# Optimization experiments

Hardware: AMD Instinct MI355X
Metric: run time of the kernel (lower is better)

The kernel has to match this reference:

```python
import jax, jax.numpy as jnp
import numpy as np

NEG_INF = float("-inf")
WINDOW = 5  # window_size in LocalAttention; half = WINDOW // 2 = 2


def setup_inputs() -> dict:
    key = jax.random.key(0)
    kq, kk, kv = jax.random.split(key, 3)
    B, L, H, E = 4, 2048, 8, 64
    queries = jax.random.normal(kq, (B, L, H, E), dtype=jnp.float32)
    keys = jax.random.normal(kk, (B, L, H, E), dtype=jnp.float32)
    values = jax.random.normal(kv, (B, L, H, E), dtype=jnp.float32)
    return {"queries": queries, "keys": keys, "values": values}


def reference(queries, keys, values):
    # queries/keys/values: [B, L, H, E]; dropout is identity (eval mode).
    B, L, H, E = queries.shape
    scale = 1.0 / jnp.sqrt(jnp.asarray(E, dtype=queries.dtype))
    # Shared scores for both branches: [B, H, L, S]
    scores = jnp.einsum("blhe,bshe->bhls", queries, keys)

    # Global (unmasked) branch
    A_global = jax.nn.softmax(scale * scores, axis=-1)

    # Local branch: torch mask allows j in [max(i-2,0), min(i+2,L)) => i-2 <= j <= i+1
    half = WINDOW // 2
    i = jnp.arange(L)[:, None]
    j = jnp.arange(L)[None, :]
    allowed = (j - i >= -half) & (j - i < half)  # [L, L], asymmetric window
    local_scores = jnp.where(allowed, scores, NEG_INF)
    A_local = jax.nn.softmax(scale * local_scores, axis=-1)

    # Sum of the two attention outputs == (A_global + A_local) @ V
    out = jnp.einsum("bhls,bshd->blhd", A_global + A_local, values)
    return out
```

## Files before the change

### kernel.cpp

```cpp
#include <hip/hip_runtime.h>
#include <hip/hip_bf16.h>
#include <stdint.h>


#define LQ 2048
#define HQ 8
#define EQ 64
#define BQ 4
#define BN 64
#define RS (HQ * EQ)
#define SCALE_LOG2E 0.18033688011112042f
#define NTILE (LQ / BN)
#define TILE_U32 2048
#define IMG_U32 (BQ * HQ * NTILE * TILE_U32)
#define BMQ 64

typedef __attribute__((ext_vector_type(8))) short bf16x8;
typedef __attribute__((ext_vector_type(4))) float f32x4;
typedef __attribute__((ext_vector_type(4))) unsigned int u32x4;
typedef __attribute__((ext_vector_type(2))) unsigned int u32x2;

static __device__ __forceinline__ unsigned int f2bf(float f) {
    union { float f; unsigned int u; } c; c.f = f;
    return (c.u + 0x8000u) >> 16;
}
static __device__ __forceinline__ unsigned int pk2(float lo, float hi) {
    union { float f; unsigned int u; } a, b; a.f = lo; b.f = hi;
    return ((a.u + 0x8000u) >> 16) | ((b.u + 0x8000u) & 0xffff0000u);
}
static __device__ __forceinline__ float fexp2(float x) {
    float r;
    asm volatile("v_exp_f32 %0, %1\n\ts_nop 1" : "=v"(r) : "v"(x));
    return r;
}

__global__ __launch_bounds__(256) void prepack_kernel(
    const float* __restrict__ K, const float* __restrict__ V,
    uint32_t* __restrict__ Kimg, uint32_t* __restrict__ Vimg)
{
    __shared__ float vf[64 * 64];

    const int tid = threadIdx.x;
    const int jc  = blockIdx.x;
    const int bh  = blockIdx.y;
    const int b   = bh >> 3;
    const int h   = bh & 7;
    const int j0  = jc * BN;
    const float* Kbh = K + (size_t)b * LQ * RS + h * EQ;
    const float* Vbh = V + (size_t)b * LQ * RS + h * EQ;
    uint32_t* Kt = Kimg + (size_t)(bh * NTILE + jc) * TILE_U32;
    uint32_t* Vt = Vimg + (size_t)(bh * NTILE + jc) * TILE_U32;

    #pragma unroll
    for (int it = 0; it < 2; ++it) {
        int t2 = tid + it * 256;
        int jr = t2 >> 3, eo = t2 & 7;
        const float* src = Kbh + (size_t)(j0 + jr) * RS + eo * 8;
        float4 a  = *(const float4*)src;
        float4 bv = *(const float4*)(src + 4);
        u32x4 p;
        p.x = pk2(a.x, a.y);   p.y = pk2(a.z, a.w);
        p.z = pk2(bv.x, bv.y); p.w = pk2(bv.z, bv.w);
        *(u32x4*)&Kt[jr * 32 + ((eo ^ (jr & 7)) << 2)] = p;
    }

    {
        const int jr = tid >> 2;
        const int s  = (jr & 7) ^ (jr >> 3);
        const float* src = Vbh + (size_t)(j0 + jr) * RS + (tid & 3) * 16;
        #pragma unroll
        for (int q = 0; q < 4; ++q) {
            float4 a = *(const float4*)(src + q * 4);
            const int ec = (tid & 3) * 4 + q;
            const int p  = (ec & 8) | ((ec ^ s) & 7);
            *(float4*)&vf[jr * 64 + p * 4] = a;
        }
    }
    __syncthreads();

    #pragma unroll
    for (int it = 0; it < 2; ++it) {
        const int u   = tid + it * 256;
        const int e   = u >> 3;
        const int jop = u & 7;
        const int jo  = jop ^ (e & 7);
        const int ec  = e >> 2;
        float v[8];
        #pragma unroll
        for (int k = 0; k < 8; ++k) {
            const int j = jo * 8 + k;
            const int p = (ec & 8) | ((ec ^ (j & 7) ^ (j >> 3)) & 7);
            v[k] = vf[j * 64 + p * 4 + (e & 3)];
        }
        u32x4 pq;
        pq.x = pk2(v[0], v[1]); pq.y = pk2(v[2], v[3]);
        pq.z = pk2(v[4], v[5]); pq.w = pk2(v[6], v[7]);
        *(u32x4*)&Vt[e * 32 + (jop << 2)] = pq;
    }
}

__global__ __launch_bounds__(256, 4) void hybrid_attn_v15(
    const float* __restrict__ Q, const float* __restrict__ K,
    const float* __restrict__ V, const uint32_t* __restrict__ Kimg,
    const uint32_t* __restrict__ Vimg, float* __restrict__ O)
{
    __shared__ unsigned short KV[8192];
    __shared__ unsigned short Pt[4][1024];
    __shared__ float sloc[BMQ][4];

    const int tid  = threadIdx.x;
    const int wave = tid >> 6;
    const int lane = tid & 63;
    const int c    = lane & 15;
    const int g    = lane >> 4;
    const int id   = blockIdx.x;
    const int bh   = (id & 7) * 4 + ((id >> 3) & 3);
    const int qt   = id >> 5;
    const int b    = bh >> 3;
    const int h    = bh & 7;
    const int i0   = qt * BMQ;
    const int c7   = c & 7;
    const int sw3  = c7 << 1;

    const float* Qbh = Q + (size_t)b * LQ * RS + h * EQ;
    const float* Kbh = K + (size_t)b * LQ * RS + h * EQ;
    const float* Vbh = V + (size_t)b * LQ * RS + h * EQ;
    float*       Obh = O + (size_t)b * LQ * RS + h * EQ;

    bf16x8 qf[2];
    {
        const int iq = i0 + wave * 16 + c;
        const float* qrow = Qbh + (size_t)iq * RS + g * 8;
        #pragma unroll
        for (int f = 0; f < 2; ++f) {
            float4 a  = *(const float4*)(qrow + f * 32);
            float4 bv = *(const float4*)(qrow + f * 32 + 4);
            union { bf16x8 v; unsigned int u[4]; } fr;
            fr.u[0] = pk2(a.x  * SCALE_LOG2E, a.y  * SCALE_LOG2E);
            fr.u[1] = pk2(a.z  * SCALE_LOG2E, a.w  * SCALE_LOG2E);
            fr.u[2] = pk2(bv.x * SCALE_LOG2E, bv.y * SCALE_LOG2E);
            fr.u[3] = pk2(bv.z * SCALE_LOG2E, bv.w * SCALE_LOG2E);
            qf[f] = fr.v;
        }
    }

    const int fo0 = c * 64 + ((g ^ c7) << 3);
    const int fo1 = c * 64 + (((4 | g) ^ c7) << 3);

    unsigned short* pw[4];
    #pragma unroll
    for (int n = 0; n < 4; ++n)
        pw[n] = &Pt[wave][c * 64 + ((((n << 2) | g) ^ sw3) << 2)];
    unsigned short* pr0 = &Pt[wave][c * 64 + (((g << 1) ^ sw3) << 2)];
    unsigned short* pr1 = &Pt[wave][c * 64 + (((8 | (g << 1)) ^ sw3) << 2)];

    const uint32_t* kgb = Kimg + (size_t)bh * (NTILE * TILE_U32) + wave * 512 + lane * 4;
    const uint32_t* vgb = Vimg + (size_t)bh * (NTILE * TILE_U32) + wave * 512 + lane * 4;

    unsigned short* kd0 = &KV[wave * 1024 + lane * 8];
    unsigned short* kd1 = &KV[wave * 1024 + 512 + lane * 8];
    unsigned short* vd0 = &KV[4096 + wave * 1024 + lane * 8];
    unsigned short* vd1 = &KV[4096 + wave * 1024 + 512 + lane * 8];

    f32x4 oacc[4];
    #pragma unroll
    for (int eg = 0; eg < 4; ++eg) oacc[eg] = (f32x4){0.f, 0.f, 0.f, 0.f};
    float lsum = 0.f;

    u32x4 kr0 = *(const u32x4*)kgb;
    u32x4 kr1 = *(const u32x4*)(kgb + 256);
    u32x4 vr0 = *(const u32x4*)vgb;
    u32x4 vr1 = *(const u32x4*)(vgb + 256);

    for (int jc = 0; jc < NTILE; ++jc) {
        __syncthreads();
        *(u32x4*)kd0 = kr0;
        *(u32x4*)kd1 = kr1;
        *(u32x4*)vd0 = vr0;
        *(u32x4*)vd1 = vr1;
        if (jc + 1 < NTILE) {
            const uint32_t* kg = kgb + (size_t)(jc + 1) * TILE_U32;
            const uint32_t* vg = vgb + (size_t)(jc + 1) * TILE_U32;
            kr0 = *(const u32x4*)kg;
            kr1 = *(const u32x4*)(kg + 256);
            vr0 = *(const u32x4*)vg;
            vr1 = *(const u32x4*)(vg + 256);
        }
        __syncthreads();

        bf16x8 kfr[4][2];
        #pragma unroll
        for (int n = 0; n < 4; ++n) {
            kfr[n][0] = *(const bf16x8*)&KV[n * 1024 + fo0];
            kfr[n][1] = *(const bf16x8*)&KV[n * 1024 + fo1];
        }

        f32x4 sf[4];
        #pragma unroll
        for (int n = 0; n < 4; ++n) {
            f32x4 acc = (f32x4){0.f, 0.f, 0.f, 0.f};
            acc = __builtin_amdgcn_mfma_f32_16x16x32_bf16(kfr[n][0], qf[0], acc, 0, 0, 0);
            acc = __builtin_amdgcn_mfma_f32_16x16x32_bf16(kfr[n][1], qf[1], acc, 0, 0, 0);
            sf[n] = acc;
        }
        float ls = 0.f;
        #pragma unroll
        for (int n = 0; n < 4; ++n) {
            float p0 = fexp2(sf[n][0]);
            float p1 = fexp2(sf[n][1]);
            float p2 = fexp2(sf[n][2]);
            float p3 = fexp2(sf[n][3]);
            ls += (p0 + p1) + (p2 + p3);
            u32x2 pkd;
            pkd.x = pk2(p0, p1);
            pkd.y = pk2(p2, p3);
            *(u32x2*)pw[n] = pkd;
        }
        lsum += ls;
        asm volatile("s_waitcnt lgkmcnt(0)" ::: "memory");

        bf16x8 pf0 = *(const bf16x8*)pr0;
        bf16x8 pf1 = *(const bf16x8*)pr1;
        #pragma unroll
        for (int eg = 0; eg < 4; ++eg) {
            bf16x8 v0 = *(const bf16x8*)&KV[4096 + eg * 1024 + fo0];
            bf16x8 v1 = *(const bf16x8*)&KV[4096 + eg * 1024 + fo1];
            oacc[eg] = __builtin_amdgcn_mfma_f32_16x16x32_bf16(v0, pf0, oacc[eg], 0, 0, 0);
            oacc[eg] = __builtin_amdgcn_mfma_f32_16x16x32_bf16(v1, pf1, oacc[eg], 0, 0, 0);
        }
    }

    float linv;
    {
        float l = lsum;
        l += __shfl_xor(l, 16);
        l += __shfl_xor(l, 32);
        linv = 1.0f / l;
    }

    {
        const int br = tid >> 2;
        const int jj = tid & 3;
        const int i  = i0 + br;
        const int j  = i - 2 + jj;
        float s = -INFINITY;
        if (j >= 0 && j < LQ) {
            const float* qrow = Qbh + (size_t)i * RS;
            const float* krow = Kbh + (size_t)j * RS;
            float acc = 0.f;
            #pragma unroll
            for (int e = 0; e < 64; e += 4) {
                float4 qa = *(const float4*)(qrow + e);
                float4 ka = *(const float4*)(krow + e);
                acc = fmaf(qa.x, ka.x, acc); acc = fmaf(qa.y, ka.y, acc);
                acc = fmaf(qa.z, ka.z, acc); acc = fmaf(qa.w, ka.w, acc);
            }
            s = 0.125f * acc;
        }
        sloc[br][jj] = s;
    }
    __syncthreads();

    {
        const int row = wave * 16 + c;
        const int i   = i0 + row;
        float s0 = sloc[row][0], s1 = sloc[row][1], s2 = sloc[row][2], s3 = sloc[row][3];
        float mx = fmaxf(fmaxf(s0, s1), fmaxf(s2, s3));
        float w0 = expf(s0 - mx), w1 = expf(s1 - mx);
        float w2 = expf(s2 - mx), w3 = expf(s3 - mx);
        float inv = 1.0f / (w0 + w1 + w2 + w3);
        w0 *= inv; w1 *= inv; w2 *= inv; w3 *= inv;
        const float li = linv;
        float* orow = Obh + (size_t)i * RS;
        #pragma unroll
        for (int eg = 0; eg < 4; ++eg) {
            const int e0 = eg * 16 + g * 4;
            float v0 = oacc[eg][0] * li;
            float v1 = oacc[eg][1] * li;
            float v2 = oacc[eg][2] * li;
            float v3 = oacc[eg][3] * li;
            if (w0 > 0.f) {
                float4 vv = *(const float4*)(Vbh + (size_t)(i - 2) * RS + e0);
                v0 = fmaf(w0, vv.x, v0); v1 = fmaf(w0, vv.y, v1);
                v2 = fmaf(w0, vv.z, v2); v3 = fmaf(w0, vv.w, v3);
            }
            if (w1 > 0.f) {
                float4 vv = *(const float4*)(Vbh + (size_t)(i - 1) * RS + e0);
                v0 = fmaf(w1, vv.x, v0); v1 = fmaf(w1, vv.y, v1);
                v2 = fmaf(w1, vv.z, v2); v3 = fmaf(w1, vv.w, v3);
            }
            {
                float4 vv = *(const float4*)(Vbh + (size_t)i * RS + e0);
                v0 = fmaf(w2, vv.x, v0); v1 = fmaf(w2, vv.y, v1);
                v2 = fmaf(w2, vv.z, v2); v3 = fmaf(w2, vv.w, v3);
            }
            if (w3 > 0.f) {
                float4 vv = *(const float4*)(Vbh + (size_t)(i + 1) * RS + e0);
                v0 = fmaf(w3, vv.x, v0); v1 = fmaf(w3, vv.y, v1);
                v2 = fmaf(w3, vv.z, v2); v3 = fmaf(w3, vv.w, v3);
            }
            float4 outv; outv.x = v0; outv.y = v1; outv.z = v2; outv.w = v3;
            *(float4*)(orow + e0) = outv;
        }
    }
}

__global__ __launch_bounds__(256) void hybrid_attn_fb(
    const float* __restrict__ Q, const float* __restrict__ K,
    const float* __restrict__ V, float* __restrict__ O)
{
    __shared__ unsigned short Ks[64 * 64];
    __shared__ unsigned short Vt[64 * 64];
    __shared__ unsigned short Ps[4][16 * 64];
    __shared__ float sloc[64][4];

    const int tid  = threadIdx.x;
    const int wave = tid >> 6;
    const int lane = tid & 63;
    const int c    = lane & 15;
    const int g    = lane >> 4;
    const int qt   = blockIdx.x;
    const int bh   = blockIdx.y;
    const int b    = bh >> 3;
    const int h    = bh & 7;
    const int i0   = qt * 64;

    const float* Qbh = Q + (size_t)b * LQ * RS + h * EQ;
    const float* Kbh = K + (size_t)b * LQ * RS + h * EQ;
    const float* Vbh = V + (size_t)b * LQ * RS + h * EQ;
    float*       Obh = O + (size_t)b * LQ * RS + h * EQ;

    bf16x8 qf[2];
    {
        const int iA = i0 + wave * 16 + c;
        const float* qrow = Qbh + (size_t)iA * RS + g * 8;
        #pragma unroll
        for (int f = 0; f < 2; ++f) {
            float4 a  = *(const float4*)(qrow + f * 32);
            float4 bv = *(const float4*)(qrow + f * 32 + 4);
            union { bf16x8 v; unsigned int u[4]; } fr;
            fr.u[0] = pk2(a.x  * SCALE_LOG2E, a.y  * SCALE_LOG2E);
            fr.u[1] = pk2(a.z  * SCALE_LOG2E, a.w  * SCALE_LOG2E);
            fr.u[2] = pk2(bv.x * SCALE_LOG2E, bv.y * SCALE_LOG2E);
            fr.u[3] = pk2(bv.z * SCALE_LOG2E, bv.w * SCALE_LOG2E);
            qf[f] = fr.v;
        }
    }

    int kfo[4][2], vfo[4][2], pfo[2], pso[4][4];
    #pragma unroll
    for (int n = 0; n < 4; ++n)
        #pragma unroll
        for (int f = 0; f < 2; ++f)
            kfo[n][f] = (n * 16 + c) * 64 + ((((f << 2) | g) ^ (c & 7)) << 3);
    #pragma unroll
    for (int eg = 0; eg < 4; ++eg)
        #pragma unroll
        for (int kh = 0; kh < 2; ++kh)
            vfo[eg][kh] = (eg * 16 + c) * 64 + ((((kh << 2) | g) ^ (c & 7)) << 3);
    #pragma unroll
    for (int kh = 0; kh < 2; ++kh)
        pfo[kh] = c * 64 + ((((kh << 2) | g) ^ (c & 7)) << 3);
    #pragma unroll
    for (int r = 0; r < 4; ++r) {
        const int row = g * 4 + r;
        #pragma unroll
        for (int n = 0; n < 4; ++n) {
            const int col = n * 16 + c;
            pso[r][n] = row * 64 + ((((col >> 3) ^ (row & 7)) << 3) | (col & 7));
        }
    }

    f32x4 oacc[4];
    #pragma unroll
    for (int eg = 0; eg < 4; ++eg) oacc[eg] = (f32x4){0.f, 0.f, 0.f, 0.f};
    float l_r[4] = {0.f, 0.f, 0.f, 0.f};

    for (int j0 = 0; j0 < LQ; j0 += BN) {
        __syncthreads();
        #pragma unroll
        for (int it = 0; it < 2; ++it) {
            int t2 = tid + it * 256;
            int jr = t2 >> 3, eo = t2 & 7;
            const float* src = Kbh + (size_t)(j0 + jr) * RS + eo * 8;
            float4 a  = *(const float4*)src;
            float4 bv = *(const float4*)(src + 4);
            u32x4 p;
            p.x = pk2(a.x, a.y);   p.y = pk2(a.z, a.w);
            p.z = pk2(bv.x, bv.y); p.w = pk2(bv.z, bv.w);
            *(u32x4*)&Ks[jr * 64 + ((eo ^ (jr & 7)) << 3)] = p;
        }
        #pragma unroll
        for (int it = 0; it < 2; ++it) {
            int t2 = tid + it * 256;
            int e = t2 & 63, jo = t2 >> 6;
            const float* src = Vbh + (size_t)(j0 + jo * 8) * RS + e;
            float v0 = src[0 * RS], v1 = src[1 * RS], v2 = src[2 * RS], v3 = src[3 * RS];
            float v4 = src[4 * RS], v5 = src[5 * RS], v6 = src[6 * RS], v7 = src[7 * RS];
            u32x4 p;
            p.x = pk2(v0, v1); p.y = pk2(v2, v3);
            p.z = pk2(v4, v5); p.w = pk2(v6, v7);
            *(u32x4*)&Vt[e * 64 + ((jo ^ (e & 7)) << 3)] = p;
        }
        __syncthreads();

        f32x4 sf[4];
        #pragma unroll
        for (int n = 0; n < 4; ++n) {
            bf16x8 k0 = *(const bf16x8*)&Ks[kfo[n][0]];
            bf16x8 k1 = *(const bf16x8*)&Ks[kfo[n][1]];
            f32x4 acc = (f32x4){0.f, 0.f, 0.f, 0.f};
            acc = __builtin_amdgcn_mfma_f32_16x16x32_bf16(qf[0], k0, acc, 0, 0, 0);
            acc = __builtin_amdgcn_mfma_f32_16x16x32_bf16(qf[1], k1, acc, 0, 0, 0);
            sf[n] = acc;
        }
        #pragma unroll
        for (int r = 0; r < 4; ++r) {
            float p0 = fexp2(sf[0][r]);
            float p1 = fexp2(sf[1][r]);
            float p2 = fexp2(sf[2][r]);
            float p3 = fexp2(sf[3][r]);
            l_r[r] += (p0 + p1) + (p2 + p3);
            Ps[wave][pso[r][0]] = (unsigned short)f2bf(p0);
            Ps[wave][pso[r][1]] = (unsigned short)f2bf(p1);
            Ps[wave][pso[r][2]] = (unsigned short)f2bf(p2);
            Ps[wave][pso[r][3]] = (unsigned short)f2bf(p3);
        }
        asm volatile("s_waitcnt lgkmcnt(0)" ::: "memory");

        bf16x8 pf0 = *(const bf16x8*)&Ps[wave][pfo[0]];
        bf16x8 pf1 = *(const bf16x8*)&Ps[wave][pfo[1]];
        #pragma unroll
        for (int eg = 0; eg < 4; ++eg) {
            bf16x8 v0 = *(const bf16x8*)&Vt[vfo[eg][0]];
            bf16x8 v1 = *(const bf16x8*)&Vt[vfo[eg][1]];
            oacc[eg] = __builtin_amdgcn_mfma_f32_16x16x32_bf16(pf0, v0, oacc[eg], 0, 0, 0);
            oacc[eg] = __builtin_amdgcn_mfma_f32_16x16x32_bf16(pf1, v1, oacc[eg], 0, 0, 0);
        }
    }

    #pragma unroll
    for (int r = 0; r < 4; ++r) {
        float l = l_r[r];
        l += __shfl_xor(l, 1);
        l += __shfl_xor(l, 2);
        l += __shfl_xor(l, 4);
        l += __shfl_xor(l, 8);
        l_r[r] = 1.0f / l;
    }

    {
        const int br = tid >> 2;
        const int jj = tid & 3;
        const int i  = i0 + br;
        const int j  = i - 2 + jj;
        float s = -INFINITY;
        if (j >= 0 && j < LQ) {
            const float* qrow = Qbh + (size_t)i * RS;
            const float* krow = Kbh + (size_t)j * RS;
            float acc = 0.f;
            #pragma unroll
            for (int e = 0; e < 64; e += 4) {
                float4 qa = *(const float4*)(qrow + e);
                float4 ka = *(const float4*)(krow + e);
                acc = fmaf(qa.x, ka.x, acc); acc = fmaf(qa.y, ka.y, acc);
                acc = fmaf(qa.z, ka.z, acc); acc = fmaf(qa.w, ka.w, acc);
            }
            s = 0.125f * acc;
        }
        sloc[br][jj] = s;
    }
    __syncthreads();

    #pragma unroll
    for (int r = 0; r < 4; ++r) {
        const int row = wave * 16 + g * 4 + r;
        const int i   = i0 + row;
        float s0 = sloc[row][0], s1 = sloc[row][1], s2 = sloc[row][2], s3 = sloc[row][3];
        float mx = fmaxf(fmaxf(s0, s1), fmaxf(s2, s3));
        float w0 = expf(s0 - mx), w1 = expf(s1 - mx);
        float w2 = expf(s2 - mx), w3 = expf(s3 - mx);
        float inv = 1.0f / (w0 + w1 + w2 + w3);
        w0 *= inv; w1 *= inv; w2 *= inv; w3 *= inv;
        const float li = l_r[r];
        float* orow = Obh + (size_t)i * RS;
        #pragma unroll
        for (int eg = 0; eg < 4; ++eg) {
            const int e = eg * 16 + c;
            float val = oacc[eg][r] * li;
            if (w0 > 0.f) val += w0 * Vbh[(size_t)(i - 2) * RS + e];
            if (w1 > 0.f) val += w1 * Vbh[(size_t)(i - 1) * RS + e];
            if (w2 > 0.f) val += w2 * Vbh[(size_t)(i    ) * RS + e];
            if (w3 > 0.f) val += w3 * Vbh[(size_t)(i + 1) * RS + e];
            orow[e] = val;
        }
    }
}

extern "C" void kernel_launch(void* const* d_in, const int* in_sizes, int n_in,
                              void* d_out, int out_size, void* d_ws, size_t ws_size,
                              hipStream_t stream) {
    (void)in_sizes; (void)n_in; (void)out_size;
    const float* Q = (const float*)d_in[0];
    const float* K = (const float*)d_in[1];
    const float* V = (const float*)d_in[2];
    float* O = (float*)d_out;
    const size_t need = (size_t)2 * IMG_U32 * 4;
    if (ws_size >= need) {
        uint32_t* Kimg = (uint32_t*)d_ws;
        uint32_t* Vimg = Kimg + IMG_U32;
        hipLaunchKernelGGL(prepack_kernel, dim3(NTILE, BQ * HQ), dim3(256), 0, stream,
                           K, V, Kimg, Vimg);
        hipLaunchKernelGGL(hybrid_attn_v15, dim3((LQ / BMQ) * BQ * HQ), dim3(256), 0, stream,
                           Q, K, V, Kimg, Vimg, O);
    } else {
        hipLaunchKernelGGL(hybrid_attn_fb, dim3(LQ / 64, BQ * HQ), dim3(256), 0, stream,
                           Q, K, V, O);
    }
}
```

Measured before the change: 154.1 us.

## Permute K row mapping so P stays in registers, dropping LDS round-trip

Changes the prepacked K tile swizzle and the per-lane K row selection so that each lane's QK^T MFMA output already has the layout needed for the B operand of the PV MFMA. The softmax probabilities are packed straight into registers instead of being written to and read back from a per-wave LDS scratch buffer, which also removes an lgkmcnt wait and frees 8 KB of shared memory. The risk is that the new row permutation must agree exactly with the V row ordering, and the K fragment reads now use more varied addresses.

```diff
diff --git a/kernel.cpp b/kernel.cpp
--- a/kernel.cpp
+++ b/kernel.cpp
@@ -61,7 +61,8 @@
         u32x4 p;
         p.x = pk2(a.x, a.y);   p.y = pk2(a.z, a.w);
         p.z = pk2(bv.x, bv.y); p.w = pk2(bv.z, bv.w);
-        *(u32x4*)&Kt[jr * 32 + ((eo ^ (jr & 7)) << 2)] = p;
+        const int s = (jr & 3) | (((jr >> 3) & 1) << 2);
+        *(u32x4*)&Kt[jr * 32 + ((eo ^ s) << 2)] = p;
     }
 
     {
@@ -99,13 +100,12 @@
     }
 }
 
-__global__ __launch_bounds__(256, 4) void hybrid_attn_v15(
+__global__ __launch_bounds__(256, 4) void hybrid_attn_v16(
     const float* __restrict__ Q, const float* __restrict__ K,
     const float* __restrict__ V, const uint32_t* __restrict__ Kimg,
     const uint32_t* __restrict__ Vimg, float* __restrict__ O)
 {
     __shared__ unsigned short KV[8192];
-    __shared__ unsigned short Pt[4][1024];
     __shared__ float sloc[BMQ][4];
 
     const int tid  = threadIdx.x;
@@ -120,7 +120,6 @@
     const int h    = bh & 7;
     const int i0   = qt * BMQ;
     const int c7   = c & 7;
-    const int sw3  = c7 << 1;
 
     const float* Qbh = Q + (size_t)b * LQ * RS + h * EQ;
     const float* Kbh = K + (size_t)b * LQ * RS + h * EQ;
@@ -144,15 +143,18 @@
         }
     }
 
-    const int fo0 = c * 64 + ((g ^ c7) << 3);
-    const int fo1 = c * 64 + (((4 | g) ^ c7) << 3);
-
-    unsigned short* pw[4];
-    #pragma unroll
-    for (int n = 0; n < 4; ++n)
-        pw[n] = &Pt[wave][c * 64 + ((((n << 2) | g) ^ sw3) << 2)];
-    unsigned short* pr0 = &Pt[wave][c * 64 + (((g << 1) ^ sw3) << 2)];
-    unsigned short* pr1 = &Pt[wave][c * 64 + (((8 | (g << 1)) ^ sw3) << 2)];
+    const int rb = ((c >> 2) << 3) + (c & 3);
+    const int ss = (c & 3) | (((c >> 2) & 1) << 2);
+    int kfo[4][2];
+    #pragma unroll
+    for (int n = 0; n < 4; ++n) {
+        const int off = ((n & 1) << 2) + ((n >> 1) << 5);
+        const int r   = rb + off;
+        kfo[n][0] = r * 64 + ((g       ^ ss) << 3);
+        kfo[n][1] = r * 64 + (((4 | g) ^ ss) << 3);
+    }
+    const int vo0 = c * 64 + ((g ^ c7) << 3);
+    const int vo1 = c * 64 + (((4 | g) ^ c7) << 3);
 
     const uint32_t* kgb = Kimg + (size_t)bh * (NTILE * TILE_U32) + wave * 512 + lane * 4;
     const uint32_t* vgb = Vimg + (size_t)bh * (NTILE * TILE_U32) + wave * 512 + lane * 4;
@@ -191,8 +193,8 @@
         bf16x8 kfr[4][2];
         #pragma unroll
         for (int n = 0; n < 4; ++n) {
-            kfr[n][0] = *(const bf16x8*)&KV[n * 1024 + fo0];
-            kfr[n][1] = *(const bf16x8*)&KV[n * 1024 + fo1];
+            kfr[n][0] = *(const bf16x8*)&KV[kfo[n][0]];
+            kfr[n][1] = *(const bf16x8*)&KV[kfo[n][1]];
         }
 
         f32x4 sf[4];
@@ -203,6 +205,8 @@
             acc = __builtin_amdgcn_mfma_f32_16x16x32_bf16(kfr[n][1], qf[1], acc, 0, 0, 0);
             sf[n] = acc;
         }
+
+        union { bf16x8 v; unsigned int u[4]; } P0, P1;
         float ls = 0.f;
         #pragma unroll
         for (int n = 0; n < 4; ++n) {
@@ -211,22 +215,21 @@
             float p2 = fexp2(sf[n][2]);
             float p3 = fexp2(sf[n][3]);
             ls += (p0 + p1) + (p2 + p3);
-            u32x2 pkd;
-            pkd.x = pk2(p0, p1);
-            pkd.y = pk2(p2, p3);
-            *(u32x2*)pw[n] = pkd;
+            const unsigned int lo = pk2(p0, p1);
+            const unsigned int hi = pk2(p2, p3);
+            if (n == 0)      { P0.u[0] = lo; P0.u[1] = hi; }
+            else if (n == 1) { P0.u[2] = lo; P0.u[3] = hi; }
+            else if (n == 2) { P1.u[0] = lo; P1.u[1] = hi; }
+            else             { P1.u[2] = lo; P1.u[3] = hi; }
         }
         lsum += ls;
-        asm volatile("s_waitcnt lgkmcnt(0)" ::: "memory");
-
-        bf16x8 pf0 = *(const bf16x8*)pr0;
-        bf16x8 pf1 = *(const bf16x8*)pr1;
+
         #pragma unroll
         for (int eg = 0; eg < 4; ++eg) {
-            bf16x8 v0 = *(const bf16x8*)&KV[4096 + eg * 1024 + fo0];
-            bf16x8 v1 = *(const bf16x8*)&KV[4096 + eg * 1024 + fo1];
-            oacc[eg] = __builtin_amdgcn_mfma_f32_16x16x32_bf16(v0, pf0, oacc[eg], 0, 0, 0);
-            oacc[eg] = __builtin_amdgcn_mfma_f32_16x16x32_bf16(v1, pf1, oacc[eg], 0, 0, 0);
+            bf16x8 v0 = *(const bf16x8*)&KV[4096 + eg * 1024 + vo0];
+            bf16x8 v1 = *(const bf16x8*)&KV[4096 + eg * 1024 + vo1];
+            oacc[eg] = __builtin_amdgcn_mfma_f32_16x16x32_bf16(v0, P0.v, oacc[eg], 0, 0, 0);
+            oacc[eg] = __builtin_amdgcn_mfma_f32_16x16x32_bf16(v1, P1.v, oacc[eg], 0, 0, 0);
         }
     }
 
@@ -511,7 +514,7 @@
         uint32_t* Vimg = Kimg + IMG_U32;
         hipLaunchKernelGGL(prepack_kernel, dim3(NTILE, BQ * HQ), dim3(256), 0, stream,
                            K, V, Kimg, Vimg);
-        hipLaunchKernelGGL(hybrid_attn_v15, dim3((LQ / BMQ) * BQ * HQ), dim3(256), 0, stream,
+        hipLaunchKernelGGL(hybrid_attn_v16, dim3((LQ / BMQ) * BQ * HQ), dim3(256), 0, stream,
                            Q, K, V, Kimg, Vimg, O);
     } else {
         hipLaunchKernelGGL(hybrid_attn_fb, dim3(LQ / 64, BQ * HQ), dim3(256), 0, stream,
```

New measurement: 148.7 us. 1.04x faster.
